# Kernel optimization log

Hardware: AMD Instinct MI355X
Metric: run time of the kernel (lower is better)

## Reference

```python
import jax, jax.numpy as jnp
import numpy as np
from jax import lax

DISP = 4   # max displacement for correlation -> 81 channels
KSZ = 3    # deform/gate conv kernel size


def conv2d(x, w, b=None):
    out = lax.conv_general_dilated(x, w, (1, 1), 'SAME',
                                   dimension_numbers=('NCHW', 'OIHW', 'NCHW'))
    if b is not None:
        out = out + b[None, :, None, None]
    return out


def correlation(x1, x2, d=DISP):
    # FlowNet-style cost volume, kernel_size=1: per-displacement channel-mean dot product.
    B, C, H, W = x1.shape
    x2p = jnp.pad(x2, ((0, 0), (0, 0), (d, d), (d, d)))
    outs = []
    for dy in range(2 * d + 1):
        for dx in range(2 * d + 1):
            shifted = lax.dynamic_slice(x2p, (0, 0, dy, dx), (B, C, H, W))
            outs.append(jnp.sum(x1 * shifted, axis=1) / C)
    return jnp.stack(outs, axis=1)  # [B, (2d+1)^2, H, W]


def bilinear_sample(img, y, x):
    # img: [B,C,H,W]; y,x: [B,H,W] float sample coords; zero padding outside.
    B, C, H, W = img.shape
    y0 = jnp.floor(y); x0 = jnp.floor(x)
    y1 = y0 + 1.0;     x1 = x0 + 1.0
    wy1 = y - y0; wx1 = x - x0
    wy0 = 1.0 - wy1; wx0 = 1.0 - wx1
    flat = img.reshape(B, C, H * W)

    def gather(yi, xi):
        valid = (yi >= 0) & (yi <= H - 1) & (xi >= 0) & (xi <= W - 1)
        yc = jnp.clip(yi, 0, H - 1).astype(jnp.int32)
        xc = jnp.clip(xi, 0, W - 1).astype(jnp.int32)
        idx = (yc * W + xc).reshape(B, 1, H * W)
        g = jnp.take_along_axis(flat, idx, axis=2).reshape(B, C, H, W)
        return g * valid.astype(img.dtype)[:, None]

    return (gather(y0, x0) * (wy0 * wx0)[:, None]
          + gather(y0, x1) * (wy0 * wx1)[:, None]
          + gather(y1, x0) * (wy1 * wx0)[:, None]
          + gather(y1, x1) * (wy1 * wx1)[:, None])


def deform_conv(img, offset, w, k=KSZ):
    # offset: [B, 2*k*k, H, W] with (dy, dx) pairs per kernel tap (row-major).
    B, C, H, W = img.shape
    pad = (k - 1) // 2
    ys = jnp.arange(H, dtype=img.dtype)[None, :, None]
    xs = jnp.arange(W, dtype=img.dtype)[None, None, :]
    out = jnp.zeros((B, w.shape[0], H, W), dtype=img.dtype)
    for kk in range(k * k):
        ky, kx = kk // k, kk % k
        y = ys + (ky - pad) + offset[:, 2 * kk]
        x = xs + (kx - pad) + offset[:, 2 * kk + 1]
        s = bilinear_sample(img, y, x)
        out = out + jnp.einsum('oc,bchw->bohw', w[:, :, ky, kx], s)
    return out


def linear_scale(x, std_multiplier=3.0):
    pos = x > 0
    cnt = jnp.sum(pos).astype(x.dtype)
    mean = jnp.sum(jnp.where(pos, x, 0.0)) / jnp.maximum(cnt, 1.0)
    var = jnp.sum(jnp.where(pos, (x - mean) ** 2, 0.0)) / jnp.maximum(cnt - 1.0, 1.0)
    ub = mean + std_multiplier * jnp.sqrt(var)
    ub = jnp.where(cnt >= 2.0, ub, 1.0)  # matches torch nan / empty-positive fallback
    return jnp.clip(x, 0.0, lax.stop_gradient(ub)) / ub


def setup_inputs() -> dict:
    key = jax.random.key(0)
    ks = jax.random.split(key, 10)
    B, C, H, W = 8, 256, 64, 64
    f = jnp.float32
    inp = {
        'inputs':   jax.random.normal(ks[0], (B, C, H, W), f),
        'in_state': jax.random.normal(ks[1], (B, C, H, W), f),
        'w_reset':  jax.random.normal(ks[2], (C, 2 * C, 3, 3), f) * 0.02,
        'b_reset':  jnp.zeros((C,), f),
        'w_update': jax.random.normal(ks[3], (C, 2 * C, 3, 3), f) * 0.02,
        'b_update': jnp.zeros((C,), f),
        'w_out':    jax.random.normal(ks[4], (C, 2 * C, 3, 3), f) * 0.02,
        'b_out':    jnp.zeros((C,), f),
        'w_offset': jax.random.normal(ks[5], (18, 81, 1, 1), f) * 0.01,
        'w_align':  jax.random.normal(ks[6], (C, C, 3, 3), f) * 0.01,
    }
    return inp


def reference(inputs, in_state, w_reset, b_reset, w_update, b_update,
              w_out, b_out, w_offset, w_align):
    # align_features: correlation -> 1x1 offset conv -> deformable conv
    corr = correlation(inputs, in_state)
    offset = conv2d(corr, w_offset)
    aligned = deform_conv(in_state, offset, w_align)
    # ConvGRU gates with linear-scaled relu gates
    stacked = jnp.concatenate([inputs, aligned], axis=1)
    update = linear_scale(jax.nn.relu(conv2d(stacked, w_update, b_update)))
    reset = linear_scale(jax.nn.relu(conv2d(stacked, w_reset, b_reset)))
    out_in = jax.nn.relu(conv2d(jnp.concatenate([inputs, in_state * reset], axis=1), w_out, b_out))
    new_state = in_state * (1.0 - update) + out_in * update
    return (new_state, new_state)  # (out_feat, new_state)
```

## Files before the change

### kernel.cpp

```cpp
#include <hip/hip_runtime.h>
#include <stdint.h>
#include <math.h>

typedef unsigned short u16;
typedef short bf16x8 __attribute__((ext_vector_type(8)));
typedef float f32x4 __attribute__((ext_vector_type(4)));

#define MFMA16x16x32(a,b,c) __builtin_amdgcn_mfma_f32_16x16x32_bf16((a),(b),(c),0,0,0)

typedef __attribute__((address_space(3))) void as3_void;
typedef const __attribute__((address_space(1))) void as1_void;

__device__ __forceinline__ void g2l16(const void* g, void* l){
#if __has_builtin(__builtin_amdgcn_global_load_lds)
  __builtin_amdgcn_global_load_lds((as1_void*)g, (as3_void*)l, 16, 0, 0);
#else
  *(int4*)l = *(const int4*)g;
#endif
}

__device__ __forceinline__ u16 f2bf(float f){
  uint32_t u = __builtin_bit_cast(uint32_t, f);
  u += 0x7fffu + ((u >> 16) & 1u);
  return (u16)(u >> 16);
}
__device__ __forceinline__ float bf2f(u16 h){
  uint32_t u = ((uint32_t)h) << 16;
  return __builtin_bit_cast(float, u);
}
__device__ __forceinline__ void unpack8(int4 v, float* o){
  uint32_t w0=(uint32_t)v.x, w1=(uint32_t)v.y, w2=(uint32_t)v.z, w3=(uint32_t)v.w;
  o[0]=__builtin_bit_cast(float, w0<<16); o[1]=__builtin_bit_cast(float, w0&0xffff0000u);
  o[2]=__builtin_bit_cast(float, w1<<16); o[3]=__builtin_bit_cast(float, w1&0xffff0000u);
  o[4]=__builtin_bit_cast(float, w2<<16); o[5]=__builtin_bit_cast(float, w2&0xffff0000u);
  o[6]=__builtin_bit_cast(float, w3<<16); o[7]=__builtin_bit_cast(float, w3&0xffff0000u);
}
__device__ __forceinline__ int iclampi(int v,int lo,int hi){ return v<lo?lo:(v>hi?hi:v); }

__global__ void k_repack(const float* __restrict__ w_reset, const float* __restrict__ b_reset,
                         const float* __restrict__ w_update, const float* __restrict__ b_update,
                         const float* __restrict__ w_out, const float* __restrict__ w_offset,
                         const float* __restrict__ w_align,
                         u16* __restrict__ wgate, u16* __restrict__ wout,
                         u16* __restrict__ walign, float* __restrict__ woff,
                         float* __restrict__ biascat){
  int idx = blockIdx.x * 256 + threadIdx.x;
  if (idx < 512*4608){
    int e = idx & 7, j = (idx >> 3) & 2047, chunk = idx >> 14;
    int nb = chunk & 1, kk = chunk >> 1;
    int l = j & 15, q = (j >> 4) & 3, t16 = (j >> 6) & 15, ks2 = j >> 10;
    int n = nb*256 + t16*16 + l;
    int tap = kk >> 3, ksin = kk & 7;
    int c = ksin*64 + ks2*32 + q*8 + e;
    int ky = tap/3, kx = tap%3;
    float v = (n < 256) ? w_update[((n*512 + c)*3 + ky)*3 + kx]
                        : w_reset[(((n-256)*512 + c)*3 + ky)*3 + kx];
    wgate[idx] = f2bf(v);
  }
  if (idx < 256*4608){
    int e = idx & 7, j = (idx >> 3) & 1023, chunk = idx >> 13;
    int nb = chunk & 1, kk = chunk >> 1;
    int l = j & 15, q = (j >> 4) & 3, t8 = (j >> 6) & 7, ks2 = j >> 9;
    int n = nb*128 + t8*16 + l;
    int tap = kk >> 3, ksin = kk & 7;
    int c = ksin*64 + ks2*32 + q*8 + e;
    int ky = tap/3, kx = tap%3;
    wout[idx] = f2bf(w_out[((n*512 + c)*3 + ky)*3 + kx]);
  }
  if (idx < 256*2304){
    int n = idx / 2304, k = idx % 2304;
    int tap = k >> 8, c = k & 255;
    int ky = tap/3, kx = tap%3;
    walign[idx] = f2bf(w_align[((n*256 + c)*3 + ky)*3 + kx]);
  }
  if (idx < 1458) woff[idx] = w_offset[idx] * (1.f/256.f);
  if (idx < 512) biascat[idx] = (idx < 256) ? b_update[idx] : b_reset[idx-256];
}

__global__ __launch_bounds__(256) void k_transform(const float* __restrict__ inputs,
    const float* __restrict__ in_state, u16* __restrict__ stacked,
    u16* __restrict__ stacked2, u16* __restrict__ x2pad){
  __shared__ u16 t1[64*264];
  __shared__ u16 t2[64*264];
  int tid = threadIdx.x, bh = blockIdx.x;
  int b = bh >> 6, h = bh & 63;
  int w = tid & 63, cq = tid >> 6;
  for (int i = 0; i < 64; ++i){
    int c = i*4 + cq;
    int gi = ((b*256 + c)*64 + h)*64 + w;
    t1[w*264 + c] = f2bf(inputs[gi]);
    t2[w*264 + c] = f2bf(in_state[gi]);
  }
  __syncthreads();
  int px = tid >> 2, cg = tid & 3;
#pragma unroll
  for (int u = 0; u < 8; ++u){
    int c = cg*64 + u*8;
    int4 v1 = *(const int4*)(t1 + px*264 + c);
    int4 v2 = *(const int4*)(t2 + px*264 + c);
    *(int4*)(stacked  + (((b*66 + h+1)*66) + (px+1))*512 + c) = v1;
    *(int4*)(stacked2 + (((b*66 + h+1)*66) + (px+1))*512 + c) = v1;
    *(int4*)(x2pad    + (((b*72 + h+4)*72) + (px+4))*256 + c) = v2;
  }
}

__global__ __launch_bounds__(256) void k_corr(const u16* __restrict__ stacked,
    const u16* __restrict__ x2pad, float* __restrict__ corr){
  __shared__ u16 lA[8192];
  __shared__ u16 lB[32768];
  int tid = threadIdx.x, idx = blockIdx.x;
  int b = idx >> 6, ty = (idx >> 3) & 7, tx = idx & 7;
  int h0 = ty*8, w0 = tx*8;
  int wave = tid >> 6, lane = tid & 63, l15 = lane & 15, quad = lane >> 4;
  f32x4 acc[4][4];
#pragma unroll
  for (int i=0;i<4;i++)
#pragma unroll
    for (int j=0;j<4;j++){ f32x4 z = {0.f,0.f,0.f,0.f}; acc[i][j] = z; }

  for (int s = 0; s < 2; ++s){
#pragma unroll
    for (int i = 0; i < 4; ++i){
      int j = tid + i*256;
      int ml = j & 15, q = (j>>4)&3, mt = (j>>6)&3, ks = j >> 8;
      int px = mt*16 + ml, py = px >> 3, pxx = px & 7;
      const u16* g = stacked + (((b*66 + h0+py+1)*66) + (w0+pxx+1))*512 + s*128 + ks*32 + q*8;
      g2l16(g, lA + j*8);
    }
#pragma unroll
    for (int i = 0; i < 16; ++i){
      int j = tid + i*256;
      int nl = j & 15, q = (j>>4)&3, nt = (j>>6)&15, ks = j >> 10;
      int qp = nt*16 + nl, qy = qp >> 4, qx = qp & 15;
      const u16* g = x2pad + (((b*72 + h0+qy)*72) + (w0+qx))*256 + s*128 + ks*32 + q*8;
      g2l16(g, lB + j*8);
    }
    __syncthreads();
#pragma unroll
    for (int ks = 0; ks < 4; ++ks){
      bf16x8 bv[4];
#pragma unroll
      for (int ni=0; ni<4; ++ni){
        int nt = wave*4 + ni;
        bv[ni] = *(const bf16x8*)(lB + (((ks*16 + nt)*4 + quad)*16 + l15)*8);
      }
#pragma unroll
      for (int mi=0; mi<4; ++mi){
        bf16x8 av = *(const bf16x8*)(lA + (((ks*4 + mi)*4 + quad)*16 + l15)*8);
#pragma unroll
        for (int ni=0; ni<4; ++ni) acc[mi][ni] = MFMA16x16x32(av, bv[ni], acc[mi][ni]);
      }
    }
    __syncthreads();
  }
#pragma unroll
  for (int mi=0; mi<4; ++mi){
#pragma unroll
    for (int ni=0; ni<4; ++ni){
      int n = wave*64 + ni*16 + l15;
      int qy = n >> 4, qx = n & 15;
#pragma unroll
      for (int r=0; r<4; ++r){
        int m = mi*16 + quad*4 + r;
        int py = m >> 3, pxx = m & 7;
        int dy = qy - py, dx = qx - pxx;
        if ((unsigned)dy <= 8u && (unsigned)dx <= 8u)
          corr[(((b*64 + h0+py)*64) + (w0+pxx))*81 + dy*9 + dx] = acc[mi][ni][r];
      }
    }
  }
}

__global__ __launch_bounds__(256) void k_offset(const float* __restrict__ corr,
    const float* __restrict__ woff, float* __restrict__ offs){
  __shared__ float lc[32*84];
  __shared__ float lw[18*84];
  int tid = threadIdx.x, blk = blockIdx.x;
  int row = blk >> 1, half = blk & 1;
  int base = row*5184 + half*32*81;
  for (int i = tid; i < 32*81; i += 256){
    int px = i / 81, d = i % 81;
    lc[px*84 + d] = corr[base + i];
  }
  for (int i = tid; i < 18*84; i += 256){
    int o = i / 84, d = i % 84;
    if (d < 81) lw[i] = woff[o*81 + d];
  }
  __syncthreads();
  int px = tid & 31, og = tid >> 5;
  for (int o = og; o < 18; o += 8){
    float s = 0.f;
#pragma unroll
    for (int dd = 0; dd < 20; ++dd){
      float4 a = *(const float4*)(lc + px*84 + dd*4);
      float4 wv = *(const float4*)(lw + o*84 + dd*4);
      s += a.x*wv.x + a.y*wv.y + a.z*wv.z + a.w*wv.w;
    }
    s += lc[px*84 + 80] * lw[o*84 + 80];
    offs[(row*64 + half*32 + px)*18 + o] = s;
  }
}

__global__ __launch_bounds__(256) void k_deform(const u16* __restrict__ x2pad,
    const float* __restrict__ offs, const u16* __restrict__ walign,
    u16* __restrict__ stacked){
  __shared__ u16 lA[16384];
  int tid = threadIdx.x, bh = blockIdx.x;
  int b = bh >> 6, h = bh & 63;
  int wave = tid >> 6, lane = tid & 63, l15 = lane & 15, quad = lane >> 4;
  int px = tid >> 2, cg = tid & 3;
  int mt_s = px >> 4, ml_s = px & 15;
  f32x4 acc[4][4];
#pragma unroll
  for (int i=0;i<4;i++)
#pragma unroll
    for (int j=0;j<4;j++){ f32x4 z = {0.f,0.f,0.f,0.f}; acc[i][j] = z; }

  for (int tap = 0; tap < 9; ++tap){
    int ky = tap/3, kx = tap%3;
    float offy = offs[(bh*64 + px)*18 + 2*tap];
    float offx = offs[(bh*64 + px)*18 + 2*tap + 1];
    float y = (float)(h + ky - 1) + offy;
    float x = (float)(px + kx - 1) + offx;
    float y0f = floorf(y), x0f = floorf(x);
    float wy1 = y - y0f, wx1 = x - x0f;
    float wy0 = 1.f - wy1, wx0 = 1.f - wx1;
    int iy0 = iclampi((int)y0f, -4, 67), ix0 = iclampi((int)x0f, -4, 67);
    int iy1 = iclampi((int)y0f + 1, -4, 67), ix1 = iclampi((int)x0f + 1, -4, 67);
    const u16* p00 = x2pad + (((b*72 + iy0+4)*72) + (ix0+4))*256 + cg*64;
    const u16* p01 = x2pad + (((b*72 + iy0+4)*72) + (ix1+4))*256 + cg*64;
    const u16* p10 = x2pad + (((b*72 + iy1+4)*72) + (ix0+4))*256 + cg*64;
    const u16* p11 = x2pad + (((b*72 + iy1+4)*72) + (ix1+4))*256 + cg*64;
    float w00 = wy0*wx0, w01 = wy0*wx1, w10 = wy1*wx0, w11 = wy1*wx1;
#pragma unroll
    for (int u = 0; u < 8; ++u){
      int4 v00 = *(const int4*)(p00 + u*8);
      int4 v01 = *(const int4*)(p01 + u*8);
      int4 v10 = *(const int4*)(p10 + u*8);
      int4 v11 = *(const int4*)(p11 + u*8);
      float a00[8], a01[8], a10[8], a11[8];
      unpack8(v00,a00); unpack8(v01,a01); unpack8(v10,a10); unpack8(v11,a11);
      union { u16 h2[8]; int4 v; } R;
#pragma unroll
      for (int jj = 0; jj < 8; ++jj)
        R.h2[jj] = f2bf(w00*a00[jj] + w01*a01[jj] + w10*a10[jj] + w11*a11[jj]);
      int ch = cg*64 + u*8;
      int ks = ch >> 5, q = (ch >> 3) & 3;
      *(int4*)(lA + (((ks*4 + mt_s)*4 + q)*16 + ml_s)*8) = R.v;
    }
    __syncthreads();
#pragma unroll
    for (int ks = 0; ks < 8; ++ks){
      bf16x8 bv[4];
#pragma unroll
      for (int ni=0; ni<4; ++ni){
        int n = wave*64 + ni*16 + l15;
        bv[ni] = *(const bf16x8*)(walign + n*2304 + tap*256 + ks*32 + quad*8);
      }
#pragma unroll
      for (int mi=0; mi<4; ++mi){
        bf16x8 av = *(const bf16x8*)(lA + (((ks*4 + mi)*4 + quad)*16 + l15)*8);
#pragma unroll
        for (int ni=0; ni<4; ++ni) acc[mi][ni] = MFMA16x16x32(av, bv[ni], acc[mi][ni]);
      }
    }
    __syncthreads();
  }
#pragma unroll
  for (int mi=0; mi<4; ++mi){
#pragma unroll
    for (int ni=0; ni<4; ++ni){
      int n = wave*64 + ni*16 + l15;
#pragma unroll
      for (int r=0; r<4; ++r){
        int m = mi*16 + quad*4 + r;
        stacked[(((b*66 + h+1)*66) + (m+1))*512 + 256 + n] = f2bf(acc[mi][ni][r]);
      }
    }
  }
}

__device__ __forceinline__ void stageA_k(u16* __restrict__ dst,
    const u16* __restrict__ in, int b, int h0, int kk, int ks2, int tid){
  int tap = kk >> 3, ksin = kk & 7;
  int ky = tap/3, kx = tap - ky*3;
  const u16* abase = in + ((b*66 + h0 + ky)*66 + kx)*512 + ksin*64 + ks2*32;
#pragma unroll
  for (int i = 0; i < 2; ++i){
    int j = (ks2<<10) | (i<<9) | tid;
    int l = j & 15, q = (j >> 4) & 3, t16 = (j >> 6) & 15;
    int px = t16*16 + l, r = px >> 6, w = px & 63;
    g2l16(abase + (r*66 + w)*512 + q*8, dst + j*8);
  }
}
__device__ __forceinline__ void stageB16_k(u16* __restrict__ dst,
    const u16* __restrict__ wts, int nb, int kk, int ks2, int tid){
  const u16* wch = wts + (size_t)(kk*2 + nb) * 16384;
#pragma unroll
  for (int i = 0; i < 2; ++i){
    int j = (ks2<<10) | (i<<9) | tid;
    g2l16(wch + j*8, dst + j*8);
  }
}
__device__ __forceinline__ void stageB8_k(u16* __restrict__ dst,
    const u16* __restrict__ wts, int nb, int kk, int ks2, int tid){
  const u16* wch = wts + (size_t)(kk*2 + nb) * 8192;
  int j = (ks2<<9) | tid;
  g2l16(wch + j*8, dst + j*8);
}

#define PH16(CMH, AVC, BVC, AVN, BVN, LOADB, RA, RB, NMH, NK2, STG, EPI) do { \
  _Pragma("unroll") \
  for (int m4_=0;m4_<4;++m4_) \
    AVN[m4_] = *(const bf16x8*)((const u16*)(RA) + ((((NK2)*16 + wm*8 + (NMH)*4 + m4_)*4 + quad)*16 + l15)*8); \
  if (LOADB){ \
    _Pragma("unroll") \
    for (int ni_=0;ni_<4;++ni_) \
      BVN[ni_] = *(const bf16x8*)((const u16*)(RB) + ((((NK2)*16 + wn*4 + ni_)*4 + quad)*16 + l15)*8); \
  } \
  STG; \
  __builtin_amdgcn_sched_barrier(0); \
  __builtin_amdgcn_s_setprio(1); \
  _Pragma("unroll") \
  for (int m4_=0;m4_<4;++m4_){ \
    _Pragma("unroll") \
    for (int ni_=0;ni_<4;++ni_) \
      acc[(CMH)*4+m4_][ni_] = MFMA16x16x32(AVC[m4_], BVC[ni_], acc[(CMH)*4+m4_][ni_]); \
  } \
  __builtin_amdgcn_s_setprio(0); \
  __builtin_amdgcn_sched_barrier(0); \
  EPI; \
} while(0)

#define PH8(AVC, BVC, AVN, BVN, RA, RB, NK2, STG, EPI) do { \
  _Pragma("unroll") \
  for (int m8_=0;m8_<8;++m8_) \
    AVN[m8_] = *(const bf16x8*)((const u16*)(RA) + ((((NK2)*16 + wm*8 + m8_)*4 + quad)*16 + l15)*8); \
  _Pragma("unroll") \
  for (int ni_=0;ni_<2;++ni_) \
    BVN[ni_] = *(const bf16x8*)((const u16*)(RB) + ((((NK2)*8 + wn*2 + ni_)*4 + quad)*16 + l15)*8); \
  STG; \
  __builtin_amdgcn_sched_barrier(0); \
  __builtin_amdgcn_s_setprio(1); \
  _Pragma("unroll") \
  for (int m8_=0;m8_<8;++m8_){ \
    _Pragma("unroll") \
    for (int ni_=0;ni_<2;++ni_) \
      acc[m8_][ni_] = MFMA16x16x32(AVC[m8_], BVC[ni_], acc[m8_][ni_]); \
  } \
  __builtin_amdgcn_s_setprio(0); \
  __builtin_amdgcn_sched_barrier(0); \
  EPI; \
} while(0)

#define VMBAR(N) do { \
  if (N) { asm volatile("s_waitcnt vmcnt(" #N ")" ::: "memory"); } \
  else   { asm volatile("s_waitcnt vmcnt(0)" ::: "memory"); } \
  asm volatile("" ::: "memory"); \
  __builtin_amdgcn_s_barrier(); \
} while(0)
#define BARONLY do { asm volatile("" ::: "memory"); __builtin_amdgcn_s_barrier(); } while(0)

template<int NT, bool STATS>
__global__ __launch_bounds__(512, 2) void k_conv256(const u16* __restrict__ in,
    const u16* __restrict__ wts, const float* __restrict__ bias,
    u16* __restrict__ outp, float* __restrict__ partials){
  constexpr int NI = NT / 4;
  __shared__ u16 lA[2][16384];
  __shared__ u16 lB[2][NT*1024];

  int tid = threadIdx.x, g = blockIdx.x;
  int work = (g & 7) * 32 + (g >> 3);
  int nb = work >> 7, mt = work & 127;
  int b = mt >> 4, h0 = (mt & 15) * 4;
  int wave = tid >> 6, lane = tid & 63, l15 = lane & 15, quad = lane >> 4;
  int wm = wave & 1, wn = wave >> 1;

  f32x4 acc[8][NI];
#pragma unroll
  for (int i=0;i<8;i++)
#pragma unroll
    for (int j=0;j<NI;j++){ f32x4 z = {0.f,0.f,0.f,0.f}; acc[i][j] = z; }

  if constexpr (NT == 16){
    bf16x8 avA[4], avB[4], bvA[4], bvB[4];
    stageA_k(&lA[0][0], in, b, h0, 0, 0, tid);
    stageB16_k(&lB[0][0], wts, nb, 0, 0, tid);
    stageA_k(&lA[0][0], in, b, h0, 0, 1, tid);
    stageB16_k(&lB[0][0], wts, nb, 0, 1, tid);
    asm volatile("s_waitcnt vmcnt(4)" ::: "memory");
    asm volatile("" ::: "memory");
    __builtin_amdgcn_s_barrier();
#pragma unroll
    for (int m4_=0;m4_<4;++m4_)
      avA[m4_] = *(const bf16x8*)(&lA[0][0] + (((wm*8 + m4_)*4 + quad)*16 + l15)*8);
#pragma unroll
    for (int ni_=0;ni_<4;++ni_)
      bvA[ni_] = *(const bf16x8*)(&lB[0][0] + (((wn*4 + ni_)*4 + quad)*16 + l15)*8);

#pragma unroll 1
    for (int t = 0; t < 72; ++t){
      int d = t & 1;
      const u16* Acur = &lA[d][0];
      const u16* Bcur = &lB[d][0];
      u16* Anx = &lA[d^1][0];
      u16* Bnx = &lB[d^1][0];
      bool hn = (t < 71);
      int kn = t + 1;
      PH16(0, avA, bvA, avB, bvB, 0, Acur, Bcur, 1, 0,
           if (hn){ stageA_k(Anx, in, b, h0, kn, 0, tid);
                    stageB16_k(Bnx, wts, nb, kn, 0, tid); },
           if (hn) VMBAR(4); else VMBAR(0));
      PH16(1, avB, bvA, avA, bvB, 1, Acur, Bcur, 0, 1, , );
      PH16(0, avA, bvB, avB, bvA, 0, Acur, Bcur, 1, 1,
           if (hn){ stageA_k(Anx, in, b, h0, kn, 1, tid);
                    stageB16_k(Bnx, wts, nb, kn, 1, tid); },
           if (hn) VMBAR(4); else VMBAR(0));
      PH16(1, avB, bvB, avA, bvA, 1, Anx, Bnx, 0, 0, , BARONLY);
    }
  } else {
    bf16x8 avA[8], avB[8], bvA[2], bvB[2];
    stageA_k(&lA[0][0], in, b, h0, 0, 0, tid);
    stageB8_k(&lB[0][0], wts, nb, 0, 0, tid);
    stageA_k(&lA[0][0], in, b, h0, 0, 1, tid);
    stageB8_k(&lB[0][0], wts, nb, 0, 1, tid);
    stageA_k(&lA[1][0], in, b, h0, 1, 0, tid);
    stageB8_k(&lB[1][0], wts, nb, 1, 0, tid);
    asm volatile("s_waitcnt vmcnt(3)" ::: "memory");
    asm volatile("" ::: "memory");
    __builtin_amdgcn_s_barrier();
#pragma unroll
    for (int m8_=0;m8_<8;++m8_)
      avA[m8_] = *(const bf16x8*)(&lA[0][0] + (((wm*8 + m8_)*4 + quad)*16 + l15)*8);
#pragma unroll
    for (int ni_=0;ni_<2;++ni_)
      bvA[ni_] = *(const bf16x8*)(&lB[0][0] + (((wn*2 + ni_)*4 + quad)*16 + l15)*8);

#pragma unroll 1
    for (int t = 0; t < 72; ++t){
      int d = t & 1;
      const u16* Acur = &lA[d][0];
      const u16* Bcur = &lB[d][0];
      u16* Anx = &lA[d^1][0];
      u16* Bnx = &lB[d^1][0];
      u16* Acu = &lA[d][0];
      u16* Bcu = &lB[d][0];
      bool h1 = (t < 71), h2 = (t < 70);
      int kn = t + 1;
      PH8(avA, bvA, avB, bvB, Acur, Bcur, 1,
          if (h1){ stageA_k(Anx, in, b, h0, kn, 1, tid);
                   stageB8_k(Bnx, wts, nb, kn, 1, tid); },
          if (h1) VMBAR(3); else VMBAR(0));
      PH8(avB, bvB, avA, bvA, Anx, Bnx, 0,
          if (h2){ stageA_k(Acu, in, b, h0, t+2, 0, tid);
                   stageB8_k(Bcu, wts, nb, t+2, 0, tid); },
          if (h2) VMBAR(3); else VMBAR(0));
    }
  }

  float bvl[NI];
#pragma unroll
  for (int ni = 0; ni < NI; ++ni)
    bvl[ni] = bias[nb*(NT*16) + wn*(NI*16) + ni*16 + l15];
  float sc = 0.f, ss = 0.f, sq = 0.f;
#pragma unroll
  for (int mi=0; mi<8; ++mi){
#pragma unroll
    for (int ni=0; ni<NI; ++ni){
      int n = nb*(NT*16) + wn*(NI*16) + ni*16 + l15;
#pragma unroll
      for (int r=0; r<4; ++r){
        int m = wm*128 + mi*16 + quad*4 + r;
        int row = h0 + (m >> 6), w = m & 63;
        float v = acc[mi][ni][r] + bvl[ni];
        v = fmaxf(v, 0.f);
        outp[(((b*64 + row)*64) + w)*(NT*32) + n] = f2bf(v);
        if (STATS){ sc += (v > 0.f) ? 1.f : 0.f; ss += v; sq += v*v; }
      }
    }
  }
  if constexpr (STATS){
    __shared__ float red[8][3];
#pragma unroll
    for (int off = 32; off; off >>= 1){
      sc += __shfl_down(sc, off); ss += __shfl_down(ss, off); sq += __shfl_down(sq, off);
    }
    if (lane == 0){ red[wave][0]=sc; red[wave][1]=ss; red[wave][2]=sq; }
    __syncthreads();
    if (tid == 0){
      float a0=0,a1=0,a2=0;
      for (int w2=0; w2<8; ++w2){ a0+=red[w2][0]; a1+=red[w2][1]; a2+=red[w2][2]; }
      partials[work*3+0]=a0; partials[work*3+1]=a1; partials[work*3+2]=a2;
    }
  }
}

__global__ __launch_bounds__(256) void k_finalize(const float* __restrict__ partials,
                                                  float* __restrict__ ubs){
  __shared__ float red[4][6];
  int tid = threadIdx.x, lane = tid & 63, wave = tid >> 6;
  float cu=0,su=0,qu=0,cr=0,sr=0,qr=0;
  {
    float c = partials[tid*3+0], s = partials[tid*3+1], q = partials[tid*3+2];
    if (tid < 128){ cu=c; su=s; qu=q; } else { cr=c; sr=s; qr=q; }
  }
#pragma unroll
  for (int off = 32; off; off >>= 1){
    cu += __shfl_down(cu, off); su += __shfl_down(su, off); qu += __shfl_down(qu, off);
    cr += __shfl_down(cr, off); sr += __shfl_down(sr, off); qr += __shfl_down(qr, off);
  }
  if (lane == 0){ red[wave][0]=cu; red[wave][1]=su; red[wave][2]=qu;
                  red[wave][3]=cr; red[wave][4]=sr; red[wave][5]=qr; }
  __syncthreads();
  if (tid < 2){
    double C=0, S=0, Q=0;
    for (int w2=0; w2<4; ++w2){
      C += red[w2][tid*3+0]; S += red[w2][tid*3+1]; Q += red[w2][tid*3+2];
    }
    float ub = 1.f;
    if (C >= 2.0){
      double mean = S / C;
      double var = (Q - C*mean*mean) / (C - 1.0);
      if (var < 0.0) var = 0.0;
      ub = (float)(mean + 3.0*sqrt(var));
    }
    ubs[tid] = ub;
    ubs[2+tid] = 1.f/ub;
  }
}

__global__ __launch_bounds__(256) void k_mulreset(const u16* __restrict__ G,
    const u16* __restrict__ x2pad, const float* __restrict__ ubs,
    u16* __restrict__ stacked2){
  int tid = threadIdx.x, bh = blockIdx.x;
  int b = bh >> 6, h = bh & 63;
  int px = tid >> 2, cg = tid & 3;
  float ubr = ubs[1], inv = ubs[3];
#pragma unroll
  for (int u = 0; u < 8; ++u){
    int c = cg*64 + u*8;
    int4 gv = *(const int4*)(G + (bh*64 + px)*512 + 256 + c);
    int4 sv = *(const int4*)(x2pad + (((b*72 + h+4)*72) + (px+4))*256 + c);
    float gf[8], sf[8]; unpack8(gv, gf); unpack8(sv, sf);
    union { u16 h2[8]; int4 v; } R;
#pragma unroll
    for (int j=0;j<8;j++){
      float r = fminf(gf[j], ubr) * inv;
      R.h2[j] = f2bf(sf[j] * r);
    }
    *(int4*)(stacked2 + (((b*66 + h+1)*66) + (px+1))*512 + 256 + c) = R.v;
  }
}

__global__ __launch_bounds__(256) void k_final(const u16* __restrict__ G,
    const u16* __restrict__ O, const float* __restrict__ in_state,
    const float* __restrict__ ubs, float* __restrict__ dout){
  __shared__ float Q[64*65];
  __shared__ float P[64*65];
  int tid = threadIdx.x, bh = blockIdx.x;
  int b = bh >> 6, h = bh & 63;
  float ubu = ubs[0], inv = ubs[2];
  int px = tid >> 2, cs = (tid & 3)*16;
  int w = tid & 63, c4 = tid >> 6;
  for (int cb = 0; cb < 4; ++cb){
#pragma unroll
    for (int tt = 0; tt < 2; ++tt){
      int cl = cs + tt*8;
      int c = cb*64 + cl;
      int4 gv = *(const int4*)(G + (bh*64 + px)*512 + c);
      int4 ov = *(const int4*)(O + (bh*64 + px)*256 + c);
      float gf[8], of[8]; unpack8(gv, gf); unpack8(ov, of);
#pragma unroll
      for (int j=0;j<8;j++){
        float u = fminf(gf[j], ubu) * inv;
        Q[px*65 + cl + j] = u;
        P[px*65 + cl + j] = of[j]*u;
      }
    }
    __syncthreads();
    for (int i = 0; i < 16; ++i){
      int cl = i*4 + c4;
      int c = cb*64 + cl;
      int gidx = (((b*256 + c)*64) + h)*64 + w;
      float s = in_state[gidx];
      float v = s*(1.f - Q[w*65 + cl]) + P[w*65 + cl];
      dout[gidx] = v;
      dout[8388608 + gidx] = v;
    }
    __syncthreads();
  }
}

extern "C" void kernel_launch(void* const* d_in, const int* in_sizes, int n_in,
                              void* d_out, int out_size, void* d_ws, size_t ws_size,
                              hipStream_t stream){
  (void)in_sizes; (void)n_in; (void)out_size; (void)ws_size;
  const float* inputs   = (const float*)d_in[0];
  const float* in_state = (const float*)d_in[1];
  const float* w_reset  = (const float*)d_in[2];
  const float* b_reset  = (const float*)d_in[3];
  const float* w_update = (const float*)d_in[4];
  const float* b_update = (const float*)d_in[5];
  const float* w_out    = (const float*)d_in[6];
  const float* b_out    = (const float*)d_in[7];
  const float* w_offset = (const float*)d_in[8];
  const float* w_align  = (const float*)d_in[9];
  float* dout = (float*)d_out;

  char* ws = (char*)d_ws;
  size_t off = 0;
  auto alloc = [&](size_t bytes)->char*{
    char* p = ws + off; off = (off + bytes + 255) & ~(size_t)255; return p;
  };
  const size_t x2pad_b   = 8ull*72*72*256*2;
  const size_t stacked_b = 8ull*66*66*512*2;
  u16* x2pad    = (u16*)alloc(x2pad_b);
  u16* stacked  = (u16*)alloc(stacked_b);
  u16* stacked2 = (u16*)alloc(stacked_b);
  float* corr   = (float*)alloc(8ull*64*64*81*4);
  float* offs   = (float*)alloc(8ull*64*64*18*4);
  u16* G        = (u16*)alloc(8ull*64*64*512*2);
  u16* O        = (u16*)alloc(8ull*64*64*256*2);
  u16* wgate    = (u16*)alloc(512ull*4608*2);
  u16* woutb    = (u16*)alloc(256ull*4608*2);
  u16* walignb  = (u16*)alloc(256ull*2304*2);
  float* woff   = (float*)alloc(1458*4);
  float* biascat= (float*)alloc(512*4);
  float* partials=(float*)alloc(1024*3*4);
  float* ubs    = (float*)alloc(4*4);

  hipMemsetAsync(x2pad,    0, x2pad_b,   stream);
  hipMemsetAsync(stacked,  0, stacked_b, stream);
  hipMemsetAsync(stacked2, 0, stacked_b, stream);

  k_repack<<<9216, 256, 0, stream>>>(w_reset, b_reset, w_update, b_update, w_out,
                                     w_offset, w_align, wgate, woutb, walignb, woff, biascat);
  k_transform<<<512, 256, 0, stream>>>(inputs, in_state, stacked, stacked2, x2pad);
  k_corr<<<512, 256, 0, stream>>>(stacked, x2pad, corr);
  k_offset<<<1024, 256, 0, stream>>>(corr, woff, offs);
  k_deform<<<512, 256, 0, stream>>>(x2pad, offs, walignb, stacked);
  k_conv256<16, true><<<256, 512, 0, stream>>>(stacked, wgate, biascat, G, partials);
  k_finalize<<<1, 256, 0, stream>>>(partials, ubs);
  k_mulreset<<<512, 256, 0, stream>>>(G, x2pad, ubs, stacked2);
  k_conv256<8, false><<<256, 512, 0, stream>>>(stacked2, woutb, b_out, O, nullptr);
  k_final<<<512, 256, 0, stream>>>(G, O, in_state, ubs, dout);
}
```

Baseline: 636.2 us.

## Restructure conv main loop to one sync per tile with quarter-phase MFMA

Replaces the fine-grained vmcnt-counted barriers with a single __syncthreads per K tile. All next-tile global-to-LDS stages are now issued in the first phase. The NT=8 path is split into four quarter phases like the NT=16 path, halving the A-fragment registers, and it no longer prefetches two tiles ahead. The goals are fewer barriers and lower register pressure, at the cost of shallower prefetch and a full vmcnt(0) wait at each sync.

```diff
diff --git a/kernel.cpp b/kernel.cpp
--- a/kernel.cpp
+++ b/kernel.cpp
@@ -332,34 +332,33 @@
   EPI; \
 } while(0)
 
-#define PH8(AVC, BVC, AVN, BVN, RA, RB, NK2, STG, EPI) do { \
+#define PH8Q(CMH, AVC, BVC, AVN, BVN, LOADB, RA, RB, NMH, NK2, STG, EPI) do { \
   _Pragma("unroll") \
-  for (int m8_=0;m8_<8;++m8_) \
-    AVN[m8_] = *(const bf16x8*)((const u16*)(RA) + ((((NK2)*16 + wm*8 + m8_)*4 + quad)*16 + l15)*8); \
-  _Pragma("unroll") \
-  for (int ni_=0;ni_<2;++ni_) \
-    BVN[ni_] = *(const bf16x8*)((const u16*)(RB) + ((((NK2)*8 + wn*2 + ni_)*4 + quad)*16 + l15)*8); \
+  for (int m4_=0;m4_<4;++m4_) \
+    AVN[m4_] = *(const bf16x8*)((const u16*)(RA) + ((((NK2)*16 + wm*8 + (NMH)*4 + m4_)*4 + quad)*16 + l15)*8); \
+  if (LOADB){ \
+    _Pragma("unroll") \
+    for (int ni_=0;ni_<2;++ni_) \
+      BVN[ni_] = *(const bf16x8*)((const u16*)(RB) + ((((NK2)*8 + wn*2 + ni_)*4 + quad)*16 + l15)*8); \
+  } \
   STG; \
   __builtin_amdgcn_sched_barrier(0); \
   __builtin_amdgcn_s_setprio(1); \
   _Pragma("unroll") \
-  for (int m8_=0;m8_<8;++m8_){ \
+  for (int m4_=0;m4_<4;++m4_){ \
     _Pragma("unroll") \
     for (int ni_=0;ni_<2;++ni_) \
-      acc[m8_][ni_] = MFMA16x16x32(AVC[m8_], BVC[ni_], acc[m8_][ni_]); \
+      acc[(CMH)*4+m4_][ni_] = MFMA16x16x32(AVC[m4_], BVC[ni_], acc[(CMH)*4+m4_][ni_]); \
   } \
   __builtin_amdgcn_s_setprio(0); \
   __builtin_amdgcn_sched_barrier(0); \
   EPI; \
 } while(0)
 
-#define VMBAR(N) do { \
-  if (N) { asm volatile("s_waitcnt vmcnt(" #N ")" ::: "memory"); } \
-  else   { asm volatile("s_waitcnt vmcnt(0)" ::: "memory"); } \
-  asm volatile("" ::: "memory"); \
-  __builtin_amdgcn_s_barrier(); \
+#define SYNCTILE do { \
+  __syncthreads(); \
+  __builtin_amdgcn_sched_barrier(0); \
 } while(0)
-#define BARONLY do { asm volatile("" ::: "memory"); __builtin_amdgcn_s_barrier(); } while(0)
 
 template<int NT, bool STATS>
 __global__ __launch_bounds__(512, 2) void k_conv256(const u16* __restrict__ in,
@@ -388,9 +387,7 @@
     stageB16_k(&lB[0][0], wts, nb, 0, 0, tid);
     stageA_k(&lA[0][0], in, b, h0, 0, 1, tid);
     stageB16_k(&lB[0][0], wts, nb, 0, 1, tid);
-    asm volatile("s_waitcnt vmcnt(4)" ::: "memory");
-    asm volatile("" ::: "memory");
-    __builtin_amdgcn_s_barrier();
+    __syncthreads();
 #pragma unroll
     for (int m4_=0;m4_<4;++m4_)
       avA[m4_] = *(const bf16x8*)(&lA[0][0] + (((wm*8 + m4_)*4 + quad)*16 + l15)*8);
@@ -409,29 +406,23 @@
       int kn = t + 1;
       PH16(0, avA, bvA, avB, bvB, 0, Acur, Bcur, 1, 0,
            if (hn){ stageA_k(Anx, in, b, h0, kn, 0, tid);
-                    stageB16_k(Bnx, wts, nb, kn, 0, tid); },
-           if (hn) VMBAR(4); else VMBAR(0));
+                    stageB16_k(Bnx, wts, nb, kn, 0, tid);
+                    stageA_k(Anx, in, b, h0, kn, 1, tid);
+                    stageB16_k(Bnx, wts, nb, kn, 1, tid); }, );
       PH16(1, avB, bvA, avA, bvB, 1, Acur, Bcur, 0, 1, , );
-      PH16(0, avA, bvB, avB, bvA, 0, Acur, Bcur, 1, 1,
-           if (hn){ stageA_k(Anx, in, b, h0, kn, 1, tid);
-                    stageB16_k(Bnx, wts, nb, kn, 1, tid); },
-           if (hn) VMBAR(4); else VMBAR(0));
-      PH16(1, avB, bvB, avA, bvA, 1, Anx, Bnx, 0, 0, , BARONLY);
+      PH16(0, avA, bvB, avB, bvA, 0, Acur, Bcur, 1, 1, , SYNCTILE);
+      PH16(1, avB, bvB, avA, bvA, 1, Anx, Bnx, 0, 0, , );
     }
   } else {
-    bf16x8 avA[8], avB[8], bvA[2], bvB[2];
+    bf16x8 avA[4], avB[4], bvA[2], bvB[2];
     stageA_k(&lA[0][0], in, b, h0, 0, 0, tid);
     stageB8_k(&lB[0][0], wts, nb, 0, 0, tid);
     stageA_k(&lA[0][0], in, b, h0, 0, 1, tid);
     stageB8_k(&lB[0][0], wts, nb, 0, 1, tid);
-    stageA_k(&lA[1][0], in, b, h0, 1, 0, tid);
-    stageB8_k(&lB[1][0], wts, nb, 1, 0, tid);
-    asm volatile("s_waitcnt vmcnt(3)" ::: "memory");
-    asm volatile("" ::: "memory");
-    __builtin_amdgcn_s_barrier();
-#pragma unroll
-    for (int m8_=0;m8_<8;++m8_)
-      avA[m8_] = *(const bf16x8*)(&lA[0][0] + (((wm*8 + m8_)*4 + quad)*16 + l15)*8);
+    __syncthreads();
+#pragma unroll
+    for (int m4_=0;m4_<4;++m4_)
+      avA[m4_] = *(const bf16x8*)(&lA[0][0] + (((wm*8 + m4_)*4 + quad)*16 + l15)*8);
 #pragma unroll
     for (int ni_=0;ni_<2;++ni_)
       bvA[ni_] = *(const bf16x8*)(&lB[0][0] + (((wn*2 + ni_)*4 + quad)*16 + l15)*8);
@@ -443,18 +434,16 @@
       const u16* Bcur = &lB[d][0];
       u16* Anx = &lA[d^1][0];
       u16* Bnx = &lB[d^1][0];
-      u16* Acu = &lA[d][0];
-      u16* Bcu = &lB[d][0];
-      bool h1 = (t < 71), h2 = (t < 70);
+      bool hn = (t < 71);
       int kn = t + 1;
-      PH8(avA, bvA, avB, bvB, Acur, Bcur, 1,
-          if (h1){ stageA_k(Anx, in, b, h0, kn, 1, tid);
-                   stageB8_k(Bnx, wts, nb, kn, 1, tid); },
-          if (h1) VMBAR(3); else VMBAR(0));
-      PH8(avB, bvB, avA, bvA, Anx, Bnx, 0,
-          if (h2){ stageA_k(Acu, in, b, h0, t+2, 0, tid);
-                   stageB8_k(Bcu, wts, nb, t+2, 0, tid); },
-          if (h2) VMBAR(3); else VMBAR(0));
+      PH8Q(0, avA, bvA, avB, bvB, 0, Acur, Bcur, 1, 0,
+           if (hn){ stageA_k(Anx, in, b, h0, kn, 0, tid);
+                    stageB8_k(Bnx, wts, nb, kn, 0, tid);
+                    stageA_k(Anx, in, b, h0, kn, 1, tid);
+                    stageB8_k(Bnx, wts, nb, kn, 1, tid); }, );
+      PH8Q(1, avB, bvA, avA, bvB, 1, Acur, Bcur, 0, 1, , );
+      PH8Q(0, avA, bvB, avB, bvA, 0, Acur, Bcur, 1, 1, , SYNCTILE);
+      PH8Q(1, avB, bvB, avA, bvA, 1, Anx, Bnx, 0, 0, , );
     }
   }
 
```

After: 667.6 us. 4.9% more time.
